# Kernel tuning notes

Hardware: AMD Instinct MI355X
Metric: run time of the kernel (lower is better)

The kernel has to match this reference:

```python
import jax, jax.numpy as jnp
import numpy as np

D_MODEL = 1024
N_HEAD = 16
DIM_PER_HEAD = D_MODEL // N_HEAD
B, S = 8, 1024


def setup_inputs() -> dict:
    key = jax.random.key(0)
    ks = jax.random.split(key, 12)
    s = 0.02
    return {
        "k": jax.random.normal(ks[0], (B, S, D_MODEL), jnp.float32),
        "v": jax.random.normal(ks[1], (B, S, D_MODEL), jnp.float32),
        "q": jax.random.normal(ks[2], (B, S, D_MODEL), jnp.float32),
        "attn_mask": jax.random.randint(ks[3], (B, S, S), 0, 2, jnp.int32),
        "Wk": jax.random.normal(ks[4], (D_MODEL, D_MODEL), jnp.float32) * s,
        "bk": jnp.zeros((D_MODEL,), jnp.float32),
        "Wv": jax.random.normal(ks[5], (D_MODEL, D_MODEL), jnp.float32) * s,
        "bv": jnp.zeros((D_MODEL,), jnp.float32),
        "Wq": jax.random.normal(ks[6], (D_MODEL, D_MODEL), jnp.float32) * s,
        "bq": jnp.zeros((D_MODEL,), jnp.float32),
        "Wo": jax.random.normal(ks[7], (D_MODEL, D_MODEL), jnp.float32) * s,
        "bo": jnp.zeros((D_MODEL,), jnp.float32),
    }


def reference(k, v, q, attn_mask, Wk, bk, Wv, bv, Wq, bq, Wo, bo):
    batch, key_len, _ = k.shape
    query_len = q.shape[1]
    scale = 1.0 / jnp.sqrt(jnp.float32(DIM_PER_HEAD))

    def split_heads(x):  # [b, s, d] -> [b, h, s, dh]
        return x.reshape(batch, -1, N_HEAD, DIM_PER_HEAD).transpose(0, 2, 1, 3)

    key_up = split_heads(k @ Wk + bk)
    value_up = split_heads(v @ Wv + bv)
    query_up = split_heads(q @ Wq + bq) * scale

    # [b, h, q, k] scores; mask nonzero entries with -inf (masked_fill_ semantics)
    scores = jnp.einsum("bhqd,bhkd->bhqk", query_up, key_up)
    scores = jnp.where(attn_mask[:, None, :, :] != 0, -jnp.inf, scores)
    attn = jax.nn.softmax(scores, axis=-1)
    # NOTE: original applies dropout but discards the result; attn (pre-dropout) is used.
    context = jnp.einsum("bhqk,bhkd->bhqd", attn, value_up)
    context = context.transpose(0, 2, 1, 3).reshape(batch, query_len, D_MODEL)
    output = context @ Wo + bo
    attn_mean = attn.sum(axis=1) / N_HEAD  # [b, q, k]
    return output, attn_mean
```

## Files before the change

### kernel.cpp

```cpp
#include <hip/hip_runtime.h>
#include <hip/hip_bf16.h>

typedef unsigned short u16;
typedef unsigned int u32;
typedef __attribute__((ext_vector_type(8))) short bf16x8;
typedef __attribute__((ext_vector_type(4))) float f32x4;
typedef __attribute__((ext_vector_type(4))) u16 u16x4;
typedef __attribute__((ext_vector_type(4))) u32 u32x4;

#define DEV static __device__ __forceinline__

DEV u16 f2bf(float x) {
  unsigned u = __builtin_bit_cast(unsigned, x);
  u += 0x7fffu + ((u >> 16) & 1u);
  return (u16)(u >> 16);
}
DEV float bf2f(u16 u) { return __builtin_bit_cast(float, ((unsigned)u) << 16); }

DEV u32 cvtpk(float lo, float hi) {
  u32 r;
  asm("v_cvt_pk_bf16_f32 %0, %1, %2" : "=v"(r) : "v"(lo), "v"(hi));
  return r;
}

DEV void glds16(const u16* g, u16* l) {
  __builtin_amdgcn_global_load_lds(
      (const __attribute__((address_space(1))) void*)g,
      (__attribute__((address_space(3))) void*)l, 16, 0, 0);
}

__global__ __launch_bounds__(256) void prep(
    const float* __restrict__ k, const float* __restrict__ v,
    const float* __restrict__ q,
    const float* __restrict__ w0, const float* __restrict__ w1,
    const float* __restrict__ w2, const float* __restrict__ w3,
    const int* __restrict__ mask,
    u16* __restrict__ Xb, u16* __restrict__ WT,
    unsigned long long* __restrict__ Mb) {
  __shared__ u16 tile[32][33];
  const int bid = (int)blockIdx.x;
  const int tid = threadIdx.x;
  if (bid < 2048) {
    const size_t i0 = (size_t)bid * 256 + tid;
    for (size_t t = i0; t < 6291456; t += 524288) {
      const size_t e = t * 4;
      const float* src = (e < 8388608) ? k + e
                       : (e < 16777216) ? v + (e - 8388608)
                       : q + (e - 16777216);
      const f32x4 x = *(const f32x4*)src;
      u16x4 o;
#pragma unroll
      for (int r = 0; r < 4; ++r) o[r] = f2bf(x[r]);
      *(u16x4*)&Xb[e] = o;
    }
  } else if (bid < 6144) {
    const int lb = bid - 2048;
    const int mat = lb >> 10;
    const int bx = lb & 1023;
    const float* in = (mat == 0) ? w0 : (mat == 1) ? w1 : (mat == 2) ? w2 : w3;
    u16* o = WT + (size_t)mat * 1048576;
    const int bk = (bx & 31) << 5;
    const int bn = (bx >> 5) << 5;
    const int tx = tid & 31, ty = tid >> 5;
#pragma unroll
    for (int i = 0; i < 32; i += 8)
      tile[ty + i][tx] = f2bf(in[(size_t)(bk + ty + i) * 1024 + bn + tx]);
    __syncthreads();
#pragma unroll
    for (int i = 0; i < 32; i += 8)
      o[(size_t)(bn + ty + i) * 1024 + bk + tx] = tile[tx][ty + i];
  } else {
    const int lb = bid - 6144;
    const int qt = lb & 63, b = lb >> 6;
    const int w = tid >> 6, l = tid & 63;
    const int ln = l & 15, lg = l >> 4;
    const int* Mp = mask + ((size_t)b << 20) + ((size_t)(qt << 4) << 10);
    unsigned long long m = 0ull;
#pragma unroll
    for (int t = 0; t < 16; ++t) {
      const int key = (w << 8) + (t << 4) + ln;
#pragma unroll
      for (int r = 0; r < 4; ++r) {
        const int row = (lg << 2) + r;
        if (Mp[((size_t)row << 10) + key] != 0) m |= 1ull << ((t << 2) + r);
      }
    }
    Mb[((((size_t)b << 6) + qt) << 8) + tid] = m;
  }
}

__global__ __launch_bounds__(256) void gemm_qkv(
    const u16* __restrict__ Xb, const u16* __restrict__ WTall,
    const float* __restrict__ bK, const float* __restrict__ bV,
    const float* __restrict__ bQ,
    u16* __restrict__ Kup, u16* __restrict__ VupT, u16* __restrict__ Qup) {
  __shared__ u16 As[8192];
  __shared__ u16 Bs[8192];
  const int mode = blockIdx.y;
  const u16* A = Xb + (size_t)mode * 8388608;
  const u16* Bw = WTall + (size_t)mode * 1048576;
  const float* bias = (mode == 0) ? bK : (mode == 1) ? bV : bQ;

  const int tid = threadIdx.x;
  const int w = tid >> 6, l = tid & 63;
  const int ln = l & 15, lg = l >> 4;
  const int wr = w >> 1, wc = w & 1;
  const int bid0 = (int)blockIdx.x;
  const int sw = ((bid0 & 7) << 6) | (bid0 >> 3);
  const int mb = (sw >> 3) << 7;
  const int nb = (sw & 7) << 7;

  f32x4 acc[4][4] = {};
  const int ar = (wr << 6) + ln;
  const int br = (wc << 6) + ln;
  const int x7 = ln & 7;

  for (int k0 = 0; k0 < 1024; k0 += 64) {
#pragma unroll
    for (int i = 0; i < 4; ++i) {
      const int off = (i << 11) + (tid << 3);
      const int row = off >> 6;
      const int sc = ((((off >> 3) & 7) ^ (row & 7)) << 3);
      glds16(A + (size_t)(mb + row) * 1024 + k0 + sc, As + off);
      glds16(Bw + (size_t)(nb + row) * 1024 + k0 + sc, Bs + off);
    }
    __syncthreads();
#pragma unroll
    for (int kk = 0; kk < 2; ++kk) {
      const int g = (kk << 2) + lg;
      const int rc = (g ^ x7) << 3;
      bf16x8 aa[4], bb[4];
#pragma unroll
      for (int mt = 0; mt < 4; ++mt) {
        aa[mt] = *(const bf16x8*)&As[(ar + (mt << 4)) * 64 + rc];
        bb[mt] = *(const bf16x8*)&Bs[(br + (mt << 4)) * 64 + rc];
      }
#pragma unroll
      for (int mt = 0; mt < 4; ++mt)
#pragma unroll
        for (int nt = 0; nt < 4; ++nt)
          acc[mt][nt] = __builtin_amdgcn_mfma_f32_16x16x32_bf16(aa[mt], bb[nt], acc[mt][nt], 0, 0, 0);
    }
    __syncthreads();
  }

  const float scale = (mode == 2) ? 0.125f : 1.0f;
#pragma unroll
  for (int mt = 0; mt < 4; ++mt) {
    const int m0 = mb + (wr << 6) + (mt << 4) + (lg << 2);
    const int bb_ = m0 >> 10, s0 = m0 & 1023;
#pragma unroll
    for (int nt = 0; nt < 4; ++nt) {
      const int n = nb + (wc << 6) + (nt << 4) + ln;
      const float bval = bias[n];
      const int h = n >> 6, dh = n & 63;
      const size_t bh = (size_t)(bb_ * 16 + h);
      if (mode == 1) {
        const int wv = dh >> 4, lnv = dh & 15;
        const int kk = s0 >> 5, lgv = (s0 >> 3) & 3, e0 = s0 & 7;
        u16x4 pk;
#pragma unroll
        for (int r = 0; r < 4; ++r) pk[r] = f2bf(acc[mt][nt][r] + bval);
        *(u16x4*)&VupT[(bh << 16) + (wv << 14) + (kk << 9) + (lgv << 7) +
                       (lnv << 3) + e0] = pk;
      } else if (mode == 0) {
        const int half = dh >> 5, lg2 = (dh >> 3) & 3, e = dh & 7;
        const int T = s0 >> 4;
        u16* base = Kup + (bh << 16) + (T << 10) + (half << 9) + (lg2 << 7) + e;
#pragma unroll
        for (int r = 0; r < 4; ++r)
          base[((s0 & 15) + r) << 3] = f2bf(acc[mt][nt][r] + bval);
      } else {
#pragma unroll
        for (int r = 0; r < 4; ++r)
          Qup[((bh << 10) + s0 + r) * 64 + dh] =
              f2bf((acc[mt][nt][r] + bval) * scale);
      }
    }
  }
}

__global__ __launch_bounds__(256) void gemm_out(
    const u16* __restrict__ Ctx, const u16* __restrict__ WTall,
    const float* __restrict__ bO, const u16* __restrict__ Pp,
    float* __restrict__ Out) {
  __shared__ u16 As[8192];
  __shared__ u16 Bs[8192];
  const int bid = (int)blockIdx.x;
  const int tid = threadIdx.x;

  if (bid >= 512) {
    float* Am = Out + 8388608;
    const size_t i = ((size_t)(bid - 512) * 256 + tid) * 8;
    const u16x4* q0 = (const u16x4*)&Pp[i];
    const u16x4* q1 = (const u16x4*)&Pp[8388608 + i];
    const u16x4 a0 = q0[0], a1 = q0[1], b0 = q1[0], b1 = q1[1];
    f32x4 lo, hi;
#pragma unroll
    for (int r = 0; r < 4; ++r) {
      lo[r] = (bf2f(a0[r]) + bf2f(b0[r])) * 0.0625f;
      hi[r] = (bf2f(a1[r]) + bf2f(b1[r])) * 0.0625f;
    }
    *(f32x4*)&Am[i] = lo;
    *(f32x4*)&Am[i + 4] = hi;
    return;
  }

  const u16* Bw = WTall + 3145728;
  const int w = tid >> 6, l = tid & 63;
  const int ln = l & 15, lg = l >> 4;
  const int wr = w >> 1, wc = w & 1;
  const int sw = ((bid & 7) << 6) | (bid >> 3);
  const int mb = (sw >> 3) << 7;
  const int nb = (sw & 7) << 7;

  f32x4 acc[4][4] = {};
  const int ar = (wr << 6) + ln;
  const int br = (wc << 6) + ln;
  const int x7 = ln & 7;

  for (int k0 = 0; k0 < 1024; k0 += 64) {
#pragma unroll
    for (int i = 0; i < 4; ++i) {
      const int off = (i << 11) + (tid << 3);
      const int row = off >> 6;
      const int sc = ((((off >> 3) & 7) ^ (row & 7)) << 3);
      glds16(Ctx + (size_t)(mb + row) * 1024 + k0 + sc, As + off);
      glds16(Bw + (size_t)(nb + row) * 1024 + k0 + sc, Bs + off);
    }
    __syncthreads();
#pragma unroll
    for (int kk = 0; kk < 2; ++kk) {
      const int g = (kk << 2) + lg;
      const int rc = (g ^ x7) << 3;
      bf16x8 aa[4], bb[4];
#pragma unroll
      for (int mt = 0; mt < 4; ++mt) {
        aa[mt] = *(const bf16x8*)&As[(ar + (mt << 4)) * 64 + rc];
        bb[mt] = *(const bf16x8*)&Bs[(br + (mt << 4)) * 64 + rc];
      }
#pragma unroll
      for (int mt = 0; mt < 4; ++mt)
#pragma unroll
        for (int nt = 0; nt < 4; ++nt)
          acc[mt][nt] = __builtin_amdgcn_mfma_f32_16x16x32_bf16(aa[mt], bb[nt], acc[mt][nt], 0, 0, 0);
    }
    __syncthreads();
  }
#pragma unroll
  for (int mt = 0; mt < 4; ++mt) {
    const int m0 = mb + (wr << 6) + (mt << 4) + (lg << 2);
#pragma unroll
    for (int nt = 0; nt < 4; ++nt) {
      const int n = nb + (wc << 6) + (nt << 4) + ln;
      const float bval = bO[n];
#pragma unroll
      for (int r = 0; r < 4; ++r)
        Out[(size_t)(m0 + r) * 1024 + n] = acc[mt][nt][r] + bval;
    }
  }
}

__global__ __launch_bounds__(256, 2) void attn_kernel(
    const u16* __restrict__ Qup, const u16* __restrict__ Kf,
    const u16* __restrict__ Vf, const unsigned long long* __restrict__ Mb,
    u16* __restrict__ Ctx, u16* __restrict__ Pp) {
  __shared__ u16 P_lds[16 * 1024];
  __shared__ float red_s[4][16];
  __shared__ float invs[16];

  const int tid = threadIdx.x;
  const int w = tid >> 6, l = tid & 63;
  const int ln = l & 15, lg = l >> 4;
  const int kg8 = lg << 3;

  const int bid = (int)blockIdx.x;
  const int b = bid & 7;
  const int idx = bid >> 3;
  const int qt = idx & 63;
  const int hs = idx >> 6;
  const int qb = qt << 4;

  const unsigned long long mbits = Mb[((((size_t)b << 6) + qt) << 8) + tid];

  u32x4 accp[8];

#pragma unroll 1
  for (int hh = 0; hh < 8; ++hh) {
    const int h = (hs << 3) + hh;
    const size_t bh = (size_t)(b * 16 + h);
    const u16* Qp = Qup + ((bh << 10) + qb) * 64;
    const u16* Kb = Kf + (bh << 16);
    const u16* Vb = Vf + (bh << 16) + ((size_t)w << 14);

    const bf16x8 qa0 = *(const bf16x8*)&Qp[ln * 64 + kg8];
    const bf16x8 qa1 = *(const bf16x8*)&Qp[ln * 64 + 32 + kg8];

    bf16x8 ka[3], kb[3];
#pragma unroll
    for (int p = 0; p < 3; ++p) {
      const int To = ((w << 4) + p) << 10;
      ka[p] = *(const bf16x8*)&Kb[To + (l << 3)];
      kb[p] = *(const bf16x8*)&Kb[To + 512 + (l << 3)];
    }

    float rsum[4] = {0, 0, 0, 0};
#pragma unroll
    for (int t = 0; t < 16; ++t) {
      const int s = t % 3;
      const bf16x8 k0 = ka[s], k1 = kb[s];
      if (t + 3 < 16) {
        const int To = ((w << 4) + t + 3) << 10;
        ka[s] = *(const bf16x8*)&Kb[To + (l << 3)];
        kb[s] = *(const bf16x8*)&Kb[To + 512 + (l << 3)];
      }
      f32x4 c = {0, 0, 0, 0};
      c = __builtin_amdgcn_mfma_f32_16x16x32_bf16(qa0, k0, c, 0, 0, 0);
      c = __builtin_amdgcn_mfma_f32_16x16x32_bf16(qa1, k1, c, 0, 0, 0);
      const int key = (w << 8) + (t << 4) + ln;
      float p[4];
#pragma unroll
      for (int r = 0; r < 4; ++r) {
        p[r] = ((mbits >> ((t << 2) + r)) & 1ull) ? 0.0f : __expf(c[r] - 4.0f);
        rsum[r] += p[r];
      }
      const u32 pk01 = cvtpk(p[0], p[1]);
      const u32 pk23 = cvtpk(p[2], p[3]);
      const int r0 = lg << 2;
      *(u16*)((char*)P_lds + ((((r0 + 0) << 11) + (key << 1)) ^ (((r0 + 0) & 7) << 4))) = (u16)pk01;
      *(u16*)((char*)P_lds + ((((r0 + 1) << 11) + (key << 1)) ^ (((r0 + 1) & 7) << 4))) = (u16)(pk01 >> 16);
      *(u16*)((char*)P_lds + ((((r0 + 2) << 11) + (key << 1)) ^ (((r0 + 2) & 7) << 4))) = (u16)pk23;
      *(u16*)((char*)P_lds + ((((r0 + 3) << 11) + (key << 1)) ^ (((r0 + 3) & 7) << 4))) = (u16)(pk23 >> 16);
    }

    bf16x8 vr[4];
#pragma unroll
    for (int p = 0; p < 4; ++p)
      vr[p] = *(const bf16x8*)&Vb[(p << 9) + (l << 3)];

#pragma unroll
    for (int off = 1; off < 16; off <<= 1) {
#pragma unroll
      for (int r = 0; r < 4; ++r) rsum[r] += __shfl_xor(rsum[r], off);
    }
    if (ln == 0) {
#pragma unroll
      for (int r = 0; r < 4; ++r) red_s[w][(lg << 2) + r] = rsum[r];
    }

    __syncthreads();
    float inv[4];
#pragma unroll
    for (int r = 0; r < 4; ++r) {
      const int row = (lg << 2) + r;
      inv[r] = 1.0f / (red_s[0][row] + red_s[1][row] + red_s[2][row] + red_s[3][row]);
    }
    if (ln == 0) {
#pragma unroll
      for (int r = 0; r < 4; ++r) invs[(lg << 2) + r] = inv[r];
    }

    f32x4 c0 = {0, 0, 0, 0}, c1 = {0, 0, 0, 0};
#pragma unroll
    for (int kk = 0; kk < 32; ++kk) {
      const int s = kk & 3;
      const bf16x8 vb = vr[s];
      if (kk + 4 < 32)
        vr[s] = *(const bf16x8*)&Vb[((kk + 4) << 9) + (l << 3)];
      const int a0 = ((ln << 11) + (((kk << 5) + kg8) << 1)) ^ ((ln & 7) << 4);
      const bf16x8 pa = *(const bf16x8*)((const char*)P_lds + a0);
      if (kk & 1)
        c1 = __builtin_amdgcn_mfma_f32_16x16x32_bf16(pa, vb, c1, 0, 0, 0);
      else
        c0 = __builtin_amdgcn_mfma_f32_16x16x32_bf16(pa, vb, c0, 0, 0, 0);
    }
    {
      const u32 q01 = cvtpk((c0[0] + c1[0]) * inv[0], (c0[1] + c1[1]) * inv[1]);
      const u32 q23 = cvtpk((c0[2] + c1[2]) * inv[2], (c0[3] + c1[3]) * inv[3]);
      u16* Cp = &Ctx[(((size_t)b << 10) + qb + (lg << 2)) * 1024 + (h << 6) + (w << 4) + ln];
      Cp[0] = (u16)q01;
      Cp[1024] = (u16)(q01 >> 16);
      Cp[2048] = (u16)q23;
      Cp[3072] = (u16)(q23 >> 16);
    }

    {
      const int row = tid >> 4;
      const float iv = invs[row];
#pragma unroll
      for (int i = 0; i < 8; ++i) {
        const int chunk = (tid & 15) + (i << 4);
        const int bo_ = ((row << 11) + (chunk << 4)) ^ ((row & 7) << 4);
        const u32x4 pu = *(const u32x4*)((const char*)P_lds + bo_);
        u32x4 o;
#pragma unroll
        for (int j = 0; j < 4; ++j) {
          const float plo = __builtin_bit_cast(float, pu[j] << 16) * iv;
          const float phi = __builtin_bit_cast(float, pu[j] & 0xFFFF0000u) * iv;
          if (hh == 0) {
            o[j] = cvtpk(plo, phi);
          } else {
            const u32 a = accp[i][j];
            const float alo = __builtin_bit_cast(float, a << 16);
            const float ahi = __builtin_bit_cast(float, a & 0xFFFF0000u);
            o[j] = cvtpk(alo + plo, ahi + phi);
          }
        }
        accp[i] = o;
      }
    }
    __syncthreads();
  }

  {
    const int row = tid >> 4;
    u16* Pg = Pp + ((size_t)hs << 23) + (((size_t)b << 10) + qb + row) * 1024;
#pragma unroll
    for (int i = 0; i < 8; ++i) {
      const int chunk = (tid & 15) + (i << 4);
      *(u32x4*)&Pg[chunk << 3] = accp[i];
    }
  }
}

extern "C" void kernel_launch(void* const* d_in, const int* in_sizes, int n_in,
                              void* d_out, int out_size, void* d_ws, size_t ws_size,
                              hipStream_t stream) {
  const float* k_in = (const float*)d_in[0];
  const float* v_in = (const float*)d_in[1];
  const float* q_in = (const float*)d_in[2];
  const int* mask = (const int*)d_in[3];
  const float* Wk = (const float*)d_in[4];
  const float* bk = (const float*)d_in[5];
  const float* Wv = (const float*)d_in[6];
  const float* bv = (const float*)d_in[7];
  const float* Wq = (const float*)d_in[8];
  const float* bq = (const float*)d_in[9];
  const float* Wo = (const float*)d_in[10];
  const float* bo = (const float*)d_in[11];

  float* out = (float*)d_out;

  u16* ws = (u16*)d_ws;
  u16* WT = ws;
  u16* Xb = ws + 4194304;
  unsigned long long* Mb = (unsigned long long*)(ws + 29360128);
  u16* Pp = ws + 37748736;
  u16* Kf   = ws + 71303168;
  u16* Vf   = ws + 79691776;
  u16* Qup  = ws + 88080384;
  u16* Ctx  = ws + 96468992;

  prep<<<6656, 256, 0, stream>>>(k_in, v_in, q_in, Wk, Wv, Wq, Wo, mask,
                                 Xb, WT, Mb);
  gemm_qkv<<<dim3(512, 3), dim3(256), 0, stream>>>(
      Xb, WT, bk, bv, bq, Kf, Vf, Qup);
  attn_kernel<<<dim3(1024), dim3(256), 0, stream>>>(
      Qup, Kf, Vf, Mb, Ctx, Pp);
  gemm_out<<<4608, 256, 0, stream>>>(Ctx, WT, bo, Pp, out);
}
```

Baseline: 292.4 us.

## Merge both head-halves of attention into one 512-thread block

The attention kernel now launches 512 blocks of 512 threads instead of 1024 blocks of 256. Each block's two 256-thread groups handle the two halves of the heads, each with its own LDS P buffer and reduction arrays. This halves the block count and lets both groups share the same query tile's mask bits and scheduling. In exchange, LDS per block doubles and the launch bound changes to (512,4), which may constrain registers and occupancy.

```diff
diff --git a/kernel.cpp b/kernel.cpp
--- a/kernel.cpp
+++ b/kernel.cpp
@@ -261,33 +261,34 @@
   }
 }
 
-__global__ __launch_bounds__(256, 2) void attn_kernel(
+__global__ __launch_bounds__(512, 4) void attn_kernel(
     const u16* __restrict__ Qup, const u16* __restrict__ Kf,
     const u16* __restrict__ Vf, const unsigned long long* __restrict__ Mb,
     u16* __restrict__ Ctx, u16* __restrict__ Pp) {
-  __shared__ u16 P_lds[16 * 1024];
-  __shared__ float red_s[4][16];
-  __shared__ float invs[16];
+  __shared__ u16 P_lds[2][16384];
+  __shared__ float red_s[2][4][16];
+  __shared__ float invs[2][16];
 
   const int tid = threadIdx.x;
-  const int w = tid >> 6, l = tid & 63;
+  const int g = tid >> 8;
+  const int tidl = tid & 255;
+  const int w = tidl >> 6, l = tid & 63;
   const int ln = l & 15, lg = l >> 4;
   const int kg8 = lg << 3;
+  char* Pb = (char*)P_lds + (g << 15);
 
   const int bid = (int)blockIdx.x;
   const int b = bid & 7;
-  const int idx = bid >> 3;
-  const int qt = idx & 63;
-  const int hs = idx >> 6;
+  const int qt = bid >> 3;
   const int qb = qt << 4;
 
-  const unsigned long long mbits = Mb[((((size_t)b << 6) + qt) << 8) + tid];
+  const unsigned long long mbits = Mb[((((size_t)b << 6) + qt) << 8) + tidl];
 
   u32x4 accp[8];
 
 #pragma unroll 1
   for (int hh = 0; hh < 8; ++hh) {
-    const int h = (hs << 3) + hh;
+    const int h = (g << 3) + hh;
     const size_t bh = (size_t)(b * 16 + h);
     const u16* Qp = Qup + ((bh << 10) + qb) * 64;
     const u16* Kb = Kf + (bh << 16);
@@ -327,10 +328,10 @@
       const u32 pk01 = cvtpk(p[0], p[1]);
       const u32 pk23 = cvtpk(p[2], p[3]);
       const int r0 = lg << 2;
-      *(u16*)((char*)P_lds + ((((r0 + 0) << 11) + (key << 1)) ^ (((r0 + 0) & 7) << 4))) = (u16)pk01;
-      *(u16*)((char*)P_lds + ((((r0 + 1) << 11) + (key << 1)) ^ (((r0 + 1) & 7) << 4))) = (u16)(pk01 >> 16);
-      *(u16*)((char*)P_lds + ((((r0 + 2) << 11) + (key << 1)) ^ (((r0 + 2) & 7) << 4))) = (u16)pk23;
-      *(u16*)((char*)P_lds + ((((r0 + 3) << 11) + (key << 1)) ^ (((r0 + 3) & 7) << 4))) = (u16)(pk23 >> 16);
+      *(u16*)(Pb + ((((r0 + 0) << 11) + (key << 1)) ^ (((r0 + 0) & 7) << 4))) = (u16)pk01;
+      *(u16*)(Pb + ((((r0 + 1) << 11) + (key << 1)) ^ (((r0 + 1) & 7) << 4))) = (u16)(pk01 >> 16);
+      *(u16*)(Pb + ((((r0 + 2) << 11) + (key << 1)) ^ (((r0 + 2) & 7) << 4))) = (u16)pk23;
+      *(u16*)(Pb + ((((r0 + 3) << 11) + (key << 1)) ^ (((r0 + 3) & 7) << 4))) = (u16)(pk23 >> 16);
     }
 
     bf16x8 vr[4];
@@ -345,7 +346,7 @@
     }
     if (ln == 0) {
 #pragma unroll
-      for (int r = 0; r < 4; ++r) red_s[w][(lg << 2) + r] = rsum[r];
+      for (int r = 0; r < 4; ++r) red_s[g][w][(lg << 2) + r] = rsum[r];
     }
 
     __syncthreads();
@@ -353,11 +354,12 @@
 #pragma unroll
     for (int r = 0; r < 4; ++r) {
       const int row = (lg << 2) + r;
-      inv[r] = 1.0f / (red_s[0][row] + red_s[1][row] + red_s[2][row] + red_s[3][row]);
+      inv[r] = 1.0f / (red_s[g][0][row] + red_s[g][1][row] +
+                       red_s[g][2][row] + red_s[g][3][row]);
     }
     if (ln == 0) {
 #pragma unroll
-      for (int r = 0; r < 4; ++r) invs[(lg << 2) + r] = inv[r];
+      for (int r = 0; r < 4; ++r) invs[g][(lg << 2) + r] = inv[r];
     }
 
     f32x4 c0 = {0, 0, 0, 0}, c1 = {0, 0, 0, 0};
@@ -368,7 +370,7 @@
       if (kk + 4 < 32)
         vr[s] = *(const bf16x8*)&Vb[((kk + 4) << 9) + (l << 3)];
       const int a0 = ((ln << 11) + (((kk << 5) + kg8) << 1)) ^ ((ln & 7) << 4);
-      const bf16x8 pa = *(const bf16x8*)((const char*)P_lds + a0);
+      const bf16x8 pa = *(const bf16x8*)(Pb + a0);
       if (kk & 1)
         c1 = __builtin_amdgcn_mfma_f32_16x16x32_bf16(pa, vb, c1, 0, 0, 0);
       else
@@ -385,13 +387,13 @@
     }
 
     {
-      const int row = tid >> 4;
-      const float iv = invs[row];
+      const int row = tidl >> 4;
+      const float iv = invs[g][row];
 #pragma unroll
       for (int i = 0; i < 8; ++i) {
-        const int chunk = (tid & 15) + (i << 4);
+        const int chunk = (tidl & 15) + (i << 4);
         const int bo_ = ((row << 11) + (chunk << 4)) ^ ((row & 7) << 4);
-        const u32x4 pu = *(const u32x4*)((const char*)P_lds + bo_);
+        const u32x4 pu = *(const u32x4*)(Pb + bo_);
         u32x4 o;
 #pragma unroll
         for (int j = 0; j < 4; ++j) {
@@ -413,11 +415,11 @@
   }
 
   {
-    const int row = tid >> 4;
-    u16* Pg = Pp + ((size_t)hs << 23) + (((size_t)b << 10) + qb + row) * 1024;
+    const int row = tidl >> 4;
+    u16* Pg = Pp + ((size_t)g << 23) + (((size_t)b << 10) + qb + row) * 1024;
 #pragma unroll
     for (int i = 0; i < 8; ++i) {
-      const int chunk = (tid & 15) + (i << 4);
+      const int chunk = (tidl & 15) + (i << 4);
       *(u32x4*)&Pg[chunk << 3] = accp[i];
     }
   }
@@ -455,7 +457,7 @@
                                  Xb, WT, Mb);
   gemm_qkv<<<dim3(512, 3), dim3(256), 0, stream>>>(
       Xb, WT, bk, bv, bq, Kf, Vf, Qup);
-  attn_kernel<<<dim3(1024), dim3(256), 0, stream>>>(
+  attn_kernel<<<dim3(512), dim3(512), 0, stream>>>(
       Qup, Kf, Vf, Mb, Ctx, Pp);
   gemm_out<<<4608, 256, 0, stream>>>(Ctx, WT, bo, Pp, out);
 }
```

Result: slower. 532.8 us (+82.2%).
